# Kernel tuning notes

Measured on AMD Instinct MI355X. Metric: run time of the kernel, lower is better.

## Reference

```python
import jax, jax.numpy as jnp
import numpy as np

B, S, H, NH = 2, 2048, 2048, 16
HD = H // NH  # 128
ROPE_BASE = 10000.0


def rotate_half(x):
    x1, x2 = x[..., : x.shape[-1] // 2], x[..., x.shape[-1] // 2 :]
    return jnp.concatenate((-x2, x1), axis=-1)


def rope_cos_sin(seq_len, dim, dtype):
    inv_freq = 1.0 / (ROPE_BASE ** (jnp.arange(0, dim, 2, dtype=jnp.float32) / dim))
    t = jnp.arange(seq_len, dtype=jnp.float32)
    freqs = jnp.einsum('i,j->ij', t, inv_freq)          # [S, dim/2]
    emb = jnp.concatenate((freqs, freqs), axis=-1)       # [S, dim]
    return jnp.cos(emb).astype(dtype), jnp.sin(emb).astype(dtype)


def setup_inputs() -> dict:
    key = jax.random.key(0)
    ks = jax.random.split(key, 5)
    std = 1.0 / np.sqrt(H)
    return {
        'hidden_states': jax.random.normal(ks[0], (B, S, H), dtype=jnp.float32),
        'Wq': jax.random.normal(ks[1], (H, H), dtype=jnp.float32) * std,
        'Wk': jax.random.normal(ks[2], (H, H), dtype=jnp.float32) * std,
        'Wv': jax.random.normal(ks[3], (H, H), dtype=jnp.float32) * std,
        'Wo': jax.random.normal(ks[4], (H, H), dtype=jnp.float32) * std,
    }


def reference(hidden_states, Wq, Wk, Wv, Wo):
    bsz, q_len, _ = hidden_states.shape
    scale = 1.0 / np.sqrt(HD)
    # QKV projections (nn.Linear: x @ W.T)
    q = (hidden_states @ Wq.T).reshape(bsz, q_len, NH, HD).transpose(0, 2, 1, 3)
    k = (hidden_states @ Wk.T).reshape(bsz, q_len, NH, HD).transpose(0, 2, 1, 3)
    v = (hidden_states @ Wv.T).reshape(bsz, q_len, NH, HD).transpose(0, 2, 1, 3)
    # RoPE
    cos, sin = rope_cos_sin(q_len, HD, hidden_states.dtype)  # [S, HD]
    cos = cos[None, None]
    sin = sin[None, None]
    q = q * cos + rotate_half(q) * sin
    k = k * cos + rotate_half(k) * sin
    # attention (no mask, eval dropout = identity)
    attn = jnp.einsum('bhqd,bhkd->bhqk', q, k) * scale
    attn = jax.nn.softmax(attn.astype(jnp.float32), axis=-1).astype(q.dtype)
    out = jnp.einsum('bhqk,bhkd->bhqd', attn, v)
    out = out.transpose(0, 2, 1, 3).reshape(bsz, q_len, H)
    return out @ Wo.T
```

## Files before the change

kernel.cpp:

```cpp
#include <hip/hip_runtime.h>
#include <hip/hip_bf16.h>
#include <math.h>

#define Bb 2
#define Ss 2048
#define Hh 2048
#define NHh 16
#define HDd 128
#define Mm (Bb*Ss)

typedef __bf16 bf16;
typedef __bf16 bf16x8 __attribute__((ext_vector_type(8)));
typedef __bf16 bf16x4 __attribute__((ext_vector_type(4)));
typedef float  f32x4  __attribute__((ext_vector_type(4)));

#define MFMA16(a,b,c) __builtin_amdgcn_mfma_f32_16x16x32_bf16((a),(b),(c),0,0,0)

__device__ __forceinline__ void gll16(const void* g, void* l) {
  __builtin_amdgcn_global_load_lds((__attribute__((address_space(1))) void*)g,
                                   (__attribute__((address_space(3))) void*)l, 16, 0, 0);
}

__global__ __launch_bounds__(256) void k_tables(float* __restrict__ cosT, float* __restrict__ sinT) {
  int id = blockIdx.x * 256 + threadIdx.x;
  int s = id >> 6, j = id & 63;
  float inv = 1.0f / powf(10000.0f, (float)j * (1.0f/64.0f));
  float a = (float)s * inv;
  cosT[id] = cosf(a);
  sinT[id] = sinf(a);
}

__global__ __launch_bounds__(256) void k_cvt(const float* __restrict__ in, bf16* __restrict__ out) {
  size_t i = ((size_t)blockIdx.x * 256 + threadIdx.x) * 4;
  float4 v = *(const float4*)(in + i);
  bf16x4 r = { (bf16)v.x, (bf16)v.y, (bf16)v.z, (bf16)v.w };
  *(bf16x4*)(out + i) = r;
}

__global__ __launch_bounds__(256) void k_gemm_bt(
    const bf16* __restrict__ A, const bf16* __restrict__ Bw,
    float* __restrict__ C, int M, int N, int K)
{
  __shared__ bf16 As[128*64];
  __shared__ bf16 Bs[128*64];
  const int tid = threadIdx.x;
  const int lane = tid & 63;
  const int w = tid >> 6, wm = w & 1, wn = w >> 1;
  const int mt = M >> 7;
  const int bm = blockIdx.x % mt, bn = blockIdx.x / mt;
  const int r8 = tid >> 3, c8 = tid & 7;
  const bf16* Ag = A  + (size_t)(bm*128 + r8) * K + c8*8;
  const bf16* Bg = Bw + (size_t)(bn*128 + r8) * K + c8*8;
  bf16* Asw = &As[r8*64 + c8*8];
  bf16* Bsw = &Bs[r8*64 + c8*8];

  f32x4 acc[4][4] = {};
  for (int k0 = 0; k0 < K; k0 += 64) {
#pragma unroll
    for (int i = 0; i < 4; ++i) {
      gll16(Ag + (size_t)i*32*K + k0, Asw + i*32*64);
      gll16(Bg + (size_t)i*32*K + k0, Bsw + i*32*64);
    }
    __syncthreads();
#pragma unroll
    for (int kc = 0; kc < 2; ++kc) {
      bf16x8 af[4], bfv[4];
#pragma unroll
      for (int mi = 0; mi < 4; ++mi)
        af[mi] = *(const bf16x8*)&As[(wm*64 + mi*16 + (lane & 15))*64 + kc*32 + (lane>>4)*8];
#pragma unroll
      for (int ni = 0; ni < 4; ++ni)
        bfv[ni] = *(const bf16x8*)&Bs[(wn*64 + ni*16 + (lane & 15))*64 + kc*32 + (lane>>4)*8];
#pragma unroll
      for (int mi = 0; mi < 4; ++mi)
#pragma unroll
        for (int ni = 0; ni < 4; ++ni)
          acc[mi][ni] = MFMA16(af[mi], bfv[ni], acc[mi][ni]);
    }
    __syncthreads();
  }
#pragma unroll
  for (int mi = 0; mi < 4; ++mi)
#pragma unroll
    for (int ni = 0; ni < 4; ++ni) {
      int row0 = bm*128 + wm*64 + mi*16 + (lane>>4)*4;
      int col  = bn*128 + wn*64 + ni*16 + (lane & 15);
#pragma unroll
      for (int r = 0; r < 4; ++r)
        C[(size_t)(row0 + r) * N + col] = acc[mi][ni][r];
    }
}

__global__ __launch_bounds__(256) void k_rope(
    const float* __restrict__ Qr, const float* __restrict__ Kr,
    const float* __restrict__ cosT, const float* __restrict__ sinT,
    bf16* __restrict__ Qb, bf16* __restrict__ Kb)
{
  const size_t id = (size_t)blockIdx.x * 256 + threadIdx.x;
  const int j = (int)(id & 63);
  const size_t row = id >> 6;
  const int s = (int)((row >> 4) & (Ss - 1));
  const float c = cosT[s*64 + j], sn = sinT[s*64 + j];
  const size_t base = row * HDd;
  const float scale = 0.08838834764831845f;
  float q1 = Qr[base + j], q2 = Qr[base + 64 + j];
  float k1 = Kr[base + j], k2 = Kr[base + 64 + j];
  Qb[base + j]      = (bf16)((q1*c - q2*sn) * scale);
  Qb[base + 64 + j] = (bf16)((q2*c + q1*sn) * scale);
  Kb[base + j]      = (bf16)(k1*c - k2*sn);
  Kb[base + 64 + j] = (bf16)(k2*c + k1*sn);
}

__global__ __launch_bounds__(256) void k_transpose_v(const float* __restrict__ V, bf16* __restrict__ Vt)
{
  __shared__ float T[64][65];
  const int blk = blockIdx.x;
  const int bh = blk >> 6;
  const int rem = blk & 63;
  const int s0 = (rem >> 1) * 64, d0 = (rem & 1) * 64;
  const int b = bh >> 4, h = bh & 15;
  const int t = threadIdx.x;
#pragma unroll
  for (int i = 0; i < 4; ++i) {
    int slot = i*256 + t;
    int row = slot >> 4, c4 = slot & 15;
    float4 v = *(const float4*)(V + ((size_t)(b*Ss + s0 + row) * NHh + h) * HDd + d0 + c4*4);
    T[row][c4*4+0] = v.x; T[row][c4*4+1] = v.y; T[row][c4*4+2] = v.z; T[row][c4*4+3] = v.w;
  }
  __syncthreads();
#pragma unroll
  for (int i = 0; i < 4; ++i) {
    int slot = i*256 + t;
    int dr = slot >> 4, sc = slot & 15;
    bf16x4 r = { (bf16)T[sc*4+0][dr], (bf16)T[sc*4+1][dr],
                 (bf16)T[sc*4+2][dr], (bf16)T[sc*4+3][dr] };
    *(bf16x4*)(Vt + ((size_t)bh * HDd + d0 + dr) * Ss + s0 + sc*4) = r;
  }
}

__global__ __launch_bounds__(256) void k_attn(
    const bf16* __restrict__ Qb, const bf16* __restrict__ Kb,
    const bf16* __restrict__ Vt, bf16* __restrict__ Ob)
{
  __shared__ bf16 Ks[64*128];
  __shared__ bf16 Vs[128*64];
  __shared__ bf16 Ps[64*72];
  const int blk = blockIdx.x;
  const int bh = blk >> 5;
  const int q0 = (blk & 31) * 64;
  const int b = bh >> 4, h = bh & 15;
  const int tid = threadIdx.x, lane = tid & 63, w = tid >> 6;

  bf16x8 aq[4];
  {
    const int qr = q0 + w*16 + (lane & 15);
    const bf16* qp = Qb + ((size_t)(b*Ss + qr) * NHh + h) * HDd + (lane>>4)*8;
#pragma unroll
    for (int kc = 0; kc < 4; ++kc) aq[kc] = *(const bf16x8*)(qp + kc*32);
  }
  float m_i[4], l_i[4];
  f32x4 o[8] = {};
#pragma unroll
  for (int i = 0; i < 4; ++i) { m_i[i] = -1e30f; l_i[i] = 0.f; }

  const int rK = tid >> 4, cK = tid & 15;
  const int rV = tid >> 3, cV = tid & 7;

  for (int kv0 = 0; kv0 < Ss; kv0 += 64) {
#pragma unroll
    for (int i = 0; i < 4; ++i) {
      const int rowK = i*16 + rK; const int sck = cK ^ (rowK & 7);
      gll16(Kb + ((size_t)(b*Ss + kv0 + rowK) * NHh + h) * HDd + sck*8, &Ks[rowK*128 + cK*8]);
      const int rowV = i*32 + rV; const int scv = cV ^ (rowV & 7);
      gll16(Vt + ((size_t)bh * HDd + rowV) * Ss + kv0 + scv*8, &Vs[rowV*64 + cV*8]);
    }
    __syncthreads();

    f32x4 sf[4];
#pragma unroll
    for (int nf = 0; nf < 4; ++nf) {
      f32x4 a = {0.f,0.f,0.f,0.f};
#pragma unroll
      for (int kc = 0; kc < 4; ++kc) {
        const int row = nf*16 + (lane & 15);
        const int ch  = kc*4 + (lane>>4);
        bf16x8 bk = *(const bf16x8*)&Ks[row*128 + (ch ^ (row & 7))*8];
        a = MFMA16(aq[kc], bk, a);
      }
      sf[nf] = a;
    }
    float c_i[4];
#pragma unroll
    for (int i = 0; i < 4; ++i) {
      float x = fmaxf(fmaxf(sf[0][i], sf[1][i]), fmaxf(sf[2][i], sf[3][i]));
      x = fmaxf(x, __shfl_xor(x, 1));
      x = fmaxf(x, __shfl_xor(x, 2));
      x = fmaxf(x, __shfl_xor(x, 4));
      x = fmaxf(x, __shfl_xor(x, 8));
      float mnew = fmaxf(m_i[i], x);
      c_i[i] = __expf(m_i[i] - mnew);
      m_i[i] = mnew;
    }
    float ps[4] = {0.f,0.f,0.f,0.f};
#pragma unroll
    for (int nf = 0; nf < 4; ++nf)
#pragma unroll
      for (int i = 0; i < 4; ++i) {
        float pv = __expf(sf[nf][i] - m_i[i]);
        sf[nf][i] = pv;
        ps[i] += pv;
      }
#pragma unroll
    for (int i = 0; i < 4; ++i) {
      float s = ps[i];
      s += __shfl_xor(s, 1); s += __shfl_xor(s, 2);
      s += __shfl_xor(s, 4); s += __shfl_xor(s, 8);
      l_i[i] = l_i[i] * c_i[i] + s;
    }
#pragma unroll
    for (int nf = 0; nf < 4; ++nf)
#pragma unroll
      for (int i = 0; i < 4; ++i)
        Ps[(w*16 + (lane>>4)*4 + i)*72 + nf*16 + (lane & 15)] = (bf16)sf[nf][i];
#pragma unroll
    for (int nfo = 0; nfo < 8; ++nfo)
#pragma unroll
      for (int i = 0; i < 4; ++i)
        o[nfo][i] *= c_i[i];
#pragma unroll
    for (int kc = 0; kc < 2; ++kc) {
      bf16x8 pa = *(const bf16x8*)&Ps[(w*16 + (lane & 15))*72 + kc*32 + (lane>>4)*8];
#pragma unroll
      for (int nfo = 0; nfo < 8; ++nfo) {
        const int row = nfo*16 + (lane & 15);
        const int ch  = kc*4 + (lane>>4);
        bf16x8 bv = *(const bf16x8*)&Vs[row*64 + (ch ^ (row & 7))*8];
        o[nfo] = MFMA16(pa, bv, o[nfo]);
      }
    }
    __syncthreads();
  }
#pragma unroll
  for (int nfo = 0; nfo < 8; ++nfo)
#pragma unroll
    for (int i = 0; i < 4; ++i) {
      const int qr = q0 + w*16 + (lane>>4)*4 + i;
      const int d  = nfo*16 + (lane & 15);
      Ob[((size_t)(b*Ss + qr) * NHh + h) * HDd + d] = (bf16)(o[nfo][i] / l_i[i]);
    }
}

extern "C" void kernel_launch(void* const* d_in, const int* in_sizes, int n_in,
                              void* d_out, int out_size, void* d_ws, size_t ws_size,
                              hipStream_t stream) {
  (void)in_sizes; (void)n_in; (void)out_size; (void)ws_size;
  const float* X  = (const float*)d_in[0];
  const float* Wq = (const float*)d_in[1];
  const float* Wk = (const float*)d_in[2];
  const float* Wv = (const float*)d_in[3];
  const float* Wo = (const float*)d_in[4];
  float* out = (float*)d_out;

  char* p = (char*)d_ws;
  size_t off = 0;
  auto take = [&](size_t bytes) { char* r = p + off; off += (bytes + 255) & ~(size_t)255; return r; };

  float* cosT = (float*)take((size_t)Ss*64*4);
  float* sinT = (float*)take((size_t)Ss*64*4);
  bf16*  Xb   = (bf16*) take((size_t)Mm*Hh*2);
  bf16*  Wqb  = (bf16*) take((size_t)Hh*Hh*2);
  bf16*  Wkb  = (bf16*) take((size_t)Hh*Hh*2);
  bf16*  Wvb  = (bf16*) take((size_t)Hh*Hh*2);
  bf16*  Wob  = (bf16*) take((size_t)Hh*Hh*2);
  float* F1   = (float*)take((size_t)Mm*Hh*4);
  bf16*  Vt   = (bf16*) take((size_t)Mm*Hh*2);
  bf16*  Qb2  = (bf16*) take((size_t)Mm*Hh*2);
  bf16*  Kb2  = (bf16*) take((size_t)Mm*Hh*2);
  bf16*  Ob   = (bf16*) take((size_t)Mm*Hh*2);
  float* F2   = out;

  k_tables<<<(Ss*64)/256, 256, 0, stream>>>(cosT, sinT);
  k_cvt<<<(Mm*Hh)/4/256, 256, 0, stream>>>(X,  Xb);
  k_cvt<<<(Hh*Hh)/4/256, 256, 0, stream>>>(Wq, Wqb);
  k_cvt<<<(Hh*Hh)/4/256, 256, 0, stream>>>(Wk, Wkb);
  k_cvt<<<(Hh*Hh)/4/256, 256, 0, stream>>>(Wv, Wvb);
  k_cvt<<<(Hh*Hh)/4/256, 256, 0, stream>>>(Wo, Wob);

  const int gemm_grid = (Mm/128) * (Hh/128);
  k_gemm_bt<<<gemm_grid, 256, 0, stream>>>(Xb, Wvb, F1, Mm, Hh, Hh);
  k_transpose_v<<<(Bb*NHh)*(Ss/64)*(HDd/64), 256, 0, stream>>>(F1, Vt);
  k_gemm_bt<<<gemm_grid, 256, 0, stream>>>(Xb, Wqb, F1, Mm, Hh, Hh);
  k_gemm_bt<<<gemm_grid, 256, 0, stream>>>(Xb, Wkb, F2, Mm, Hh, Hh);
  k_rope<<<((size_t)Mm*NHh*64)/256, 256, 0, stream>>>(F1, F2, cosT, sinT, Qb2, Kb2);
  k_attn<<<Bb*NHh*(Ss/64), 256, 0, stream>>>(Qb2, Kb2, Vt, Ob);
  k_gemm_bt<<<gemm_grid, 256, 0, stream>>>(Ob, Wob, out, Mm, Hh, Hh);
}
```

Measured before the change: 556.0 us.

## Fuse QKV GEMMs with bf16/transposed epilogue, double-buffer attention, lazy softmax rescale

Concatenates Wq/Wk/Wv into one weight and runs a single QKV GEMM. Its epilogue writes Q/K in bf16 and V directly transposed, which removes the separate V transpose kernel and the fp32 intermediates. Attention now double-buffers K/V tiles in LDS and raises wave priority around the MFMA sections. Online-softmax rescaling is skipped unless the row max grows by more than 8, and both GEMM and attention get an XCD-aware block remap. The costs are Q/K now being rounded to bf16 before RoPE and double the LDS use in attention.

```diff
diff --git a/kernel.cpp b/kernel.cpp
--- a/kernel.cpp
+++ b/kernel.cpp
@@ -37,17 +37,21 @@
   *(bf16x4*)(out + i) = r;
 }
 
-__global__ __launch_bounds__(256) void k_gemm_bt(
+template<int EPI>
+__global__ __launch_bounds__(256) void k_gemm(
     const bf16* __restrict__ A, const bf16* __restrict__ Bw,
-    float* __restrict__ C, int M, int N, int K)
+    float* __restrict__ C, bf16* __restrict__ QKb, bf16* __restrict__ Vt,
+    int M, int N, int K)
 {
   __shared__ bf16 As[128*64];
   __shared__ bf16 Bs[128*64];
   const int tid = threadIdx.x;
   const int lane = tid & 63;
   const int w = tid >> 6, wm = w & 1, wn = w >> 1;
+  const int cpx = gridDim.x >> 3;
+  const int bid = (blockIdx.x & 7) * cpx + (blockIdx.x >> 3);
   const int mt = M >> 7;
-  const int bm = blockIdx.x % mt, bn = blockIdx.x / mt;
+  const int bm = bid % mt, bn = bid / mt;
   const int r8 = tid >> 3, c8 = tid & 7;
   const bf16* Ag = A  + (size_t)(bm*128 + r8) * K + c8*8;
   const bf16* Bg = Bw + (size_t)(bn*128 + r8) * K + c8*8;
@@ -79,78 +83,96 @@
     }
     __syncthreads();
   }
-#pragma unroll
-  for (int mi = 0; mi < 4; ++mi)
-#pragma unroll
-    for (int ni = 0; ni < 4; ++ni) {
-      int row0 = bm*128 + wm*64 + mi*16 + (lane>>4)*4;
-      int col  = bn*128 + wn*64 + ni*16 + (lane & 15);
-#pragma unroll
-      for (int r = 0; r < 4; ++r)
-        C[(size_t)(row0 + r) * N + col] = acc[mi][ni][r];
-    }
+  const int colB = bn*128 + wn*64;
+  if (EPI == 0) {
+#pragma unroll
+    for (int mi = 0; mi < 4; ++mi)
+#pragma unroll
+      for (int ni = 0; ni < 4; ++ni) {
+        int row0 = bm*128 + wm*64 + mi*16 + (lane>>4)*4;
+        int col  = colB + ni*16 + (lane & 15);
+#pragma unroll
+        for (int r = 0; r < 4; ++r)
+          C[(size_t)(row0 + r) * N + col] = acc[mi][ni][r];
+      }
+  } else if (colB < 4096) {
+#pragma unroll
+    for (int mi = 0; mi < 4; ++mi)
+#pragma unroll
+      for (int ni = 0; ni < 4; ++ni) {
+        int row0 = bm*128 + wm*64 + mi*16 + (lane>>4)*4;
+        int col  = colB + ni*16 + (lane & 15);
+#pragma unroll
+        for (int r = 0; r < 4; ++r)
+          QKb[(size_t)(row0 + r) * 4096 + col] = (bf16)acc[mi][ni][r];
+      }
+  } else {
+#pragma unroll
+    for (int mi = 0; mi < 4; ++mi)
+#pragma unroll
+      for (int ni = 0; ni < 4; ++ni) {
+        int row0 = bm*128 + wm*64 + mi*16 + (lane>>4)*4;
+        int n2   = colB + ni*16 + (lane & 15) - 4096;
+        int b = row0 >> 11, s0 = row0 & (Ss-1);
+        bf16x4 pk = { (bf16)acc[mi][ni][0], (bf16)acc[mi][ni][1],
+                      (bf16)acc[mi][ni][2], (bf16)acc[mi][ni][3] };
+        *(bf16x4*)&Vt[((size_t)(b*NHh + (n2>>7))*HDd + (n2&127))*Ss + s0] = pk;
+      }
+  }
 }
 
 __global__ __launch_bounds__(256) void k_rope(
-    const float* __restrict__ Qr, const float* __restrict__ Kr,
+    const bf16* __restrict__ QKb,
     const float* __restrict__ cosT, const float* __restrict__ sinT,
     bf16* __restrict__ Qb, bf16* __restrict__ Kb)
 {
   const size_t id = (size_t)blockIdx.x * 256 + threadIdx.x;
   const int j = (int)(id & 63);
   const size_t row = id >> 6;
-  const int s = (int)((row >> 4) & (Ss - 1));
+  const size_t tok = row >> 4;
+  const int h = (int)(row & 15);
+  const int s = (int)(tok & (Ss - 1));
   const float c = cosT[s*64 + j], sn = sinT[s*64 + j];
-  const size_t base = row * HDd;
+  const size_t qbase = tok * 4096 + h * 128;
   const float scale = 0.08838834764831845f;
-  float q1 = Qr[base + j], q2 = Qr[base + 64 + j];
-  float k1 = Kr[base + j], k2 = Kr[base + 64 + j];
-  Qb[base + j]      = (bf16)((q1*c - q2*sn) * scale);
-  Qb[base + 64 + j] = (bf16)((q2*c + q1*sn) * scale);
-  Kb[base + j]      = (bf16)(k1*c - k2*sn);
-  Kb[base + 64 + j] = (bf16)(k2*c + k1*sn);
-}
-
-__global__ __launch_bounds__(256) void k_transpose_v(const float* __restrict__ V, bf16* __restrict__ Vt)
-{
-  __shared__ float T[64][65];
-  const int blk = blockIdx.x;
-  const int bh = blk >> 6;
-  const int rem = blk & 63;
-  const int s0 = (rem >> 1) * 64, d0 = (rem & 1) * 64;
-  const int b = bh >> 4, h = bh & 15;
-  const int t = threadIdx.x;
-#pragma unroll
-  for (int i = 0; i < 4; ++i) {
-    int slot = i*256 + t;
-    int row = slot >> 4, c4 = slot & 15;
-    float4 v = *(const float4*)(V + ((size_t)(b*Ss + s0 + row) * NHh + h) * HDd + d0 + c4*4);
-    T[row][c4*4+0] = v.x; T[row][c4*4+1] = v.y; T[row][c4*4+2] = v.z; T[row][c4*4+3] = v.w;
-  }
-  __syncthreads();
-#pragma unroll
-  for (int i = 0; i < 4; ++i) {
-    int slot = i*256 + t;
-    int dr = slot >> 4, sc = slot & 15;
-    bf16x4 r = { (bf16)T[sc*4+0][dr], (bf16)T[sc*4+1][dr],
-                 (bf16)T[sc*4+2][dr], (bf16)T[sc*4+3][dr] };
-    *(bf16x4*)(Vt + ((size_t)bh * HDd + d0 + dr) * Ss + s0 + sc*4) = r;
-  }
+  float q1 = (float)QKb[qbase + j],        q2 = (float)QKb[qbase + 64 + j];
+  float k1 = (float)QKb[qbase + 2048 + j], k2 = (float)QKb[qbase + 2048 + 64 + j];
+  const size_t obase = row * HDd;
+  Qb[obase + j]      = (bf16)((q1*c - q2*sn) * scale);
+  Qb[obase + 64 + j] = (bf16)((q2*c + q1*sn) * scale);
+  Kb[obase + j]      = (bf16)(k1*c - k2*sn);
+  Kb[obase + 64 + j] = (bf16)(k2*c + k1*sn);
 }
 
 __global__ __launch_bounds__(256) void k_attn(
     const bf16* __restrict__ Qb, const bf16* __restrict__ Kb,
     const bf16* __restrict__ Vt, bf16* __restrict__ Ob)
 {
-  __shared__ bf16 Ks[64*128];
-  __shared__ bf16 Vs[128*64];
+  __shared__ bf16 Ks[2][64*128];
+  __shared__ bf16 Vs[2][128*64];
   __shared__ bf16 Ps[64*72];
-  const int blk = blockIdx.x;
+  const int cpx = gridDim.x >> 3;
+  const int blk = (blockIdx.x & 7) * cpx + (blockIdx.x >> 3);
   const int bh = blk >> 5;
   const int q0 = (blk & 31) * 64;
   const int b = bh >> 4, h = bh & 15;
   const int tid = threadIdx.x, lane = tid & 63, w = tid >> 6;
 
+  const int rK = tid >> 4, cK = tid & 15;
+  const int rV = tid >> 3, cV = tid & 7;
+  const bf16* Kg0 = Kb + ((size_t)b*Ss*NHh + h) * HDd;
+  const bf16* Vg0 = Vt + (size_t)bh * HDd * Ss;
+
+  auto stage = [&](int bufi, int kv0) {
+#pragma unroll
+    for (int i = 0; i < 4; ++i) {
+      const int rowK = i*16 + rK; const int sck = cK ^ (rowK & 7);
+      gll16(Kg0 + (size_t)(kv0 + rowK)*(NHh*HDd) + sck*8, &Ks[bufi][rowK*128 + cK*8]);
+      const int rowV = i*32 + rV; const int scv = cV ^ (rowV & 7);
+      gll16(Vg0 + (size_t)rowV*Ss + kv0 + scv*8, &Vs[bufi][rowV*64 + cV*8]);
+    }
+  };
+
   bf16x8 aq[4];
   {
     const int qr = q0 + w*16 + (lane & 15);
@@ -163,20 +185,18 @@
 #pragma unroll
   for (int i = 0; i < 4; ++i) { m_i[i] = -1e30f; l_i[i] = 0.f; }
 
-  const int rK = tid >> 4, cK = tid & 15;
-  const int rV = tid >> 3, cV = tid & 7;
-
-  for (int kv0 = 0; kv0 < Ss; kv0 += 64) {
-#pragma unroll
-    for (int i = 0; i < 4; ++i) {
-      const int rowK = i*16 + rK; const int sck = cK ^ (rowK & 7);
-      gll16(Kb + ((size_t)(b*Ss + kv0 + rowK) * NHh + h) * HDd + sck*8, &Ks[rowK*128 + cK*8]);
-      const int rowV = i*32 + rV; const int scv = cV ^ (rowV & 7);
-      gll16(Vt + ((size_t)bh * HDd + rowV) * Ss + kv0 + scv*8, &Vs[rowV*64 + cV*8]);
-    }
-    __syncthreads();
+  stage(0, 0);
+  asm volatile("s_waitcnt vmcnt(0)" ::: "memory");
+  __builtin_amdgcn_s_barrier();
+  asm volatile("" ::: "memory");
+
+  const int NT = Ss / 64;
+  for (int t = 0; t < NT; ++t) {
+    const int cur = t & 1;
+    if (t + 1 < NT) stage(cur ^ 1, (t + 1) * 64);
 
     f32x4 sf[4];
+    __builtin_amdgcn_s_setprio(1);
 #pragma unroll
     for (int nf = 0; nf < 4; ++nf) {
       f32x4 a = {0.f,0.f,0.f,0.f};
@@ -184,12 +204,14 @@
       for (int kc = 0; kc < 4; ++kc) {
         const int row = nf*16 + (lane & 15);
         const int ch  = kc*4 + (lane>>4);
-        bf16x8 bk = *(const bf16x8*)&Ks[row*128 + (ch ^ (row & 7))*8];
+        bf16x8 bk = *(const bf16x8*)&Ks[cur][row*128 + (ch ^ (row & 7))*8];
         a = MFMA16(aq[kc], bk, a);
       }
       sf[nf] = a;
     }
-    float c_i[4];
+    __builtin_amdgcn_s_setprio(0);
+
+    float x4[4];
 #pragma unroll
     for (int i = 0; i < 4; ++i) {
       float x = fmaxf(fmaxf(sf[0][i], sf[1][i]), fmaxf(sf[2][i], sf[3][i]));
@@ -197,9 +219,19 @@
       x = fmaxf(x, __shfl_xor(x, 2));
       x = fmaxf(x, __shfl_xor(x, 4));
       x = fmaxf(x, __shfl_xor(x, 8));
-      float mnew = fmaxf(m_i[i], x);
-      c_i[i] = __expf(m_i[i] - mnew);
-      m_i[i] = mnew;
+      x4[i] = x;
+    }
+    bool grow = (x4[0] > m_i[0] + 8.f) || (x4[1] > m_i[1] + 8.f) ||
+                (x4[2] > m_i[2] + 8.f) || (x4[3] > m_i[3] + 8.f);
+    if (__any(grow)) {
+#pragma unroll
+      for (int i = 0; i < 4; ++i) {
+        float mnew = fmaxf(m_i[i], x4[i]);
+        float c = __expf(m_i[i] - mnew);
+        m_i[i] = mnew; l_i[i] *= c;
+#pragma unroll
+        for (int nfo = 0; nfo < 8; ++nfo) o[nfo][i] *= c;
+      }
     }
     float ps[4] = {0.f,0.f,0.f,0.f};
 #pragma unroll
@@ -215,18 +247,15 @@
       float s = ps[i];
       s += __shfl_xor(s, 1); s += __shfl_xor(s, 2);
       s += __shfl_xor(s, 4); s += __shfl_xor(s, 8);
-      l_i[i] = l_i[i] * c_i[i] + s;
+      l_i[i] += s;
     }
 #pragma unroll
     for (int nf = 0; nf < 4; ++nf)
 #pragma unroll
       for (int i = 0; i < 4; ++i)
         Ps[(w*16 + (lane>>4)*4 + i)*72 + nf*16 + (lane & 15)] = (bf16)sf[nf][i];
-#pragma unroll
-    for (int nfo = 0; nfo < 8; ++nfo)
-#pragma unroll
-      for (int i = 0; i < 4; ++i)
-        o[nfo][i] *= c_i[i];
+
+    __builtin_amdgcn_s_setprio(1);
 #pragma unroll
     for (int kc = 0; kc < 2; ++kc) {
       bf16x8 pa = *(const bf16x8*)&Ps[(w*16 + (lane & 15))*72 + kc*32 + (lane>>4)*8];
@@ -234,12 +263,17 @@
       for (int nfo = 0; nfo < 8; ++nfo) {
         const int row = nfo*16 + (lane & 15);
         const int ch  = kc*4 + (lane>>4);
-        bf16x8 bv = *(const bf16x8*)&Vs[row*64 + (ch ^ (row & 7))*8];
+        bf16x8 bv = *(const bf16x8*)&Vs[cur][row*64 + (ch ^ (row & 7))*8];
         o[nfo] = MFMA16(pa, bv, o[nfo]);
       }
     }
-    __syncthreads();
+    __builtin_amdgcn_s_setprio(0);
+
+    asm volatile("s_waitcnt vmcnt(0)" ::: "memory");
+    __builtin_amdgcn_s_barrier();
+    asm volatile("" ::: "memory");
   }
+
 #pragma unroll
   for (int nfo = 0; nfo < 8; ++nfo)
 #pragma unroll
@@ -268,30 +302,23 @@
   float* cosT = (float*)take((size_t)Ss*64*4);
   float* sinT = (float*)take((size_t)Ss*64*4);
   bf16*  Xb   = (bf16*) take((size_t)Mm*Hh*2);
-  bf16*  Wqb  = (bf16*) take((size_t)Hh*Hh*2);
-  bf16*  Wkb  = (bf16*) take((size_t)Hh*Hh*2);
-  bf16*  Wvb  = (bf16*) take((size_t)Hh*Hh*2);
+  bf16*  Wqkv = (bf16*) take((size_t)3*Hh*Hh*2);
   bf16*  Wob  = (bf16*) take((size_t)Hh*Hh*2);
-  float* F1   = (float*)take((size_t)Mm*Hh*4);
+  bf16*  QKb  = (bf16*) take((size_t)Mm*4096*2);
   bf16*  Vt   = (bf16*) take((size_t)Mm*Hh*2);
-  bf16*  Qb2  = (bf16*) take((size_t)Mm*Hh*2);
+  bf16*  Qb   = (bf16*) take((size_t)Mm*Hh*2);
   bf16*  Kb2  = (bf16*) take((size_t)Mm*Hh*2);
   bf16*  Ob   = (bf16*) take((size_t)Mm*Hh*2);
-  float* F2   = out;
 
   k_tables<<<(Ss*64)/256, 256, 0, stream>>>(cosT, sinT);
   k_cvt<<<(Mm*Hh)/4/256, 256, 0, stream>>>(X,  Xb);
-  k_cvt<<<(Hh*Hh)/4/256, 256, 0, stream>>>(Wq, Wqb);
-  k_cvt<<<(Hh*Hh)/4/256, 256, 0, stream>>>(Wk, Wkb);
-  k_cvt<<<(Hh*Hh)/4/256, 256, 0, stream>>>(Wv, Wvb);
+  k_cvt<<<(Hh*Hh)/4/256, 256, 0, stream>>>(Wq, Wqkv);
+  k_cvt<<<(Hh*Hh)/4/256, 256, 0, stream>>>(Wk, Wqkv + (size_t)Hh*Hh);
+  k_cvt<<<(Hh*Hh)/4/256, 256, 0, stream>>>(Wv, Wqkv + (size_t)2*Hh*Hh);
   k_cvt<<<(Hh*Hh)/4/256, 256, 0, stream>>>(Wo, Wob);
 
-  const int gemm_grid = (Mm/128) * (Hh/128);
-  k_gemm_bt<<<gemm_grid, 256, 0, stream>>>(Xb, Wvb, F1, Mm, Hh, Hh);
-  k_transpose_v<<<(Bb*NHh)*(Ss/64)*(HDd/64), 256, 0, stream>>>(F1, Vt);
-  k_gemm_bt<<<gemm_grid, 256, 0, stream>>>(Xb, Wqb, F1, Mm, Hh, Hh);
-  k_gemm_bt<<<gemm_grid, 256, 0, stream>>>(Xb, Wkb, F2, Mm, Hh, Hh);
-  k_rope<<<((size_t)Mm*NHh*64)/256, 256, 0, stream>>>(F1, F2, cosT, sinT, Qb2, Kb2);
-  k_attn<<<Bb*NHh*(Ss/64), 256, 0, stream>>>(Qb2, Kb2, Vt, Ob);
-  k_gemm_bt<<<gemm_grid, 256, 0, stream>>>(Ob, Wob, out, Mm, Hh, Hh);
-}
+  k_gemm<1><<<(Mm/128) * (3*Hh/128), 256, 0, stream>>>(Xb, Wqkv, nullptr, QKb, Vt, Mm, 3*Hh, Hh);
+  k_rope<<<((size_t)Mm*NHh*64)/256, 256, 0, stream>>>(QKb, cosT, sinT, Qb, Kb2);
+  k_attn<<<Bb*NHh*(Ss/64), 256, 0, stream>>>(Qb, Kb2, Vt, Ob);
+  k_gemm<0><<<(Mm/128) * (Hh/128), 256, 0, stream>>>(Ob, Wob, out, nullptr, nullptr, Mm, Hh, Hh);
+}
```

After: 534.8 us. 3.8% less time.
